# Performance work log

Measured on AMD Instinct MI355X. Metric: run time of the kernel, lower is better.

The kernel has to match this reference:

```python
import jax, jax.numpy as jnp
import numpy as np

KERNEL_SIZE = 5


def setup_inputs() -> dict:
    key = jax.random.key(0)
    k1, k2 = jax.random.split(key)
    x = jax.random.normal(k1, (4, 32, 256, 256), dtype=jnp.float32)
    kernel = jax.random.normal(k2, (4, KERNEL_SIZE * KERNEL_SIZE, 256, 256), dtype=jnp.float32)
    return {"x": x, "kernel": kernel}


def reference(x, kernel):
    k = KERNEL_SIZE
    b, kk, h, w = kernel.shape
    # softmax over the k*k dim (original permutes to channels-last then softmax dim=-1)
    kern = jax.nn.softmax(jnp.transpose(kernel, (0, 2, 3, 1)), axis=-1)  # [b,h,w,k*k]
    pad = (k - 1) // 2
    # replicate padding on spatial dims
    xp = jnp.pad(x, ((0, 0), (0, 0), (pad, pad), (pad, pad)), mode="edge")
    # unfold: patch index order is di*k + dj (height offset first), matching torch unfold(2).unfold(3)
    patches = jnp.stack(
        [xp[:, :, i:i + h, j:j + w] for i in range(k) for j in range(k)], axis=-1
    )  # [b,c,h,w,k*k]
    # per-pixel softmax-weighted local sum; kernel broadcast over channel dim
    out = jnp.sum(patches * kern[:, None, :, :, :], axis=-1)  # [b,c,h,w]
    return out
```

## Files before the change

### kernel.cpp

```cpp
#include <hip/hip_runtime.h>

#define HW    256
#define HW2   (HW*HW)
#define KTAPS 25
#define TW    32
#define TH    4
#define LW    36
#define LH    8
#define NEL   (LW*LH)
#define NSTG  5
#define BUFSZ (NSTG*64)
#define NRING 4
#define DEPTH 2
#define CPB   8
#define C     32

__device__ __forceinline__ void stage(const float* __restrict__ src, float* dst,
                                      const int* __restrict__ soff) {
#pragma unroll
    for (int k = 0; k < NSTG; ++k)
        __builtin_amdgcn_global_load_lds(
            (const __attribute__((address_space(1))) unsigned int*)(src + soff[k]),
            (__attribute__((address_space(3))) unsigned int*)(dst + k * 64),
            4, 0, 0);
}

__global__ __launch_bounds__(64, 5) void ddown_kernel(
    const float* __restrict__ x,
    const float* __restrict__ kern,
    float* __restrict__ out)
{
    __shared__ __align__(16) float xt[NRING][BUFSZ];

    const int lane = threadIdx.x;
    const int txq  = lane & 15;
    const int ty   = lane >> 4;
    const int w0   = blockIdx.x * TW;
    const int h0   = blockIdx.y * TH;
    const int b    = blockIdx.z >> 2;
    const int c0   = (blockIdx.z & 3) * CPB;

    const int h = h0 + ty;
    const int w = w0 + txq * 2;

    const float* xb = x + (size_t)(b * C + c0) * HW2;

    int soff[NSTG];
#pragma unroll
    for (int k = 0; k < NSTG; ++k) {
        int idx = lane + k * 64;
        int i   = idx / LW;
        int j   = idx - i * LW;
        int hh  = min(max(h0 + i - 2, 0), HW - 1);
        int ww  = min(max(w0 + j - 2, 0), HW - 1);
        soff[k] = hh * HW + ww;
    }

    stage(xb,       xt[0], soff);
    stage(xb + HW2, xt[1], soff);

    const float* kb = kern + (size_t)b * KTAPS * HW2 + h * HW + w;
    float2 wt[KTAPS];
    float sx = 0.f, sy = 0.f;
#pragma unroll
    for (int j = 0; j < KTAPS; ++j) {
        float2 v = *(const float2*)(kb + (size_t)j * HW2);
        v.x = __expf(v.x); v.y = __expf(v.y);
        sx += v.x; sy += v.y;
        wt[j] = v;
    }
    const float ix = 1.f / sx, iy = 1.f / sy;

    float* ob = out + (size_t)(b * C + c0) * HW2 + h * HW + w;

#pragma unroll
    for (int cc = 0; cc < CPB; ++cc) {
        if (cc + DEPTH < CPB) stage(xb + (size_t)(cc + DEPTH) * HW2, xt[(cc + DEPTH) % NRING], soff);

        if (cc < 6)       asm volatile("s_waitcnt vmcnt(10)" ::: "memory");
        else if (cc == 6) asm volatile("s_waitcnt vmcnt(5)"  ::: "memory");
        else              asm volatile("s_waitcnt vmcnt(0)"  ::: "memory");

        const float* xc = xt[cc % NRING];
        float ax = 0.f, ay = 0.f;
#pragma unroll
        for (int di = 0; di < 5; ++di) {
            const float* row = &xc[(ty + di) * LW + txq * 2];
            float2 pa = *(const float2*)(row);
            float2 pb = *(const float2*)(row + 2);
            float2 pc = *(const float2*)(row + 4);
            float w6[6] = {pa.x, pa.y, pb.x, pb.y, pc.x, pc.y};
#pragma unroll
            for (int dj = 0; dj < 5; ++dj) {
                float2 wv = wt[di * 5 + dj];
                ax += wv.x * w6[dj + 0];
                ay += wv.y * w6[dj + 1];
            }
        }
        float2 res = { ax * ix, ay * iy };
        *(float2*)(ob + (size_t)cc * HW2) = res;
    }
}

extern "C" void kernel_launch(void* const* d_in, const int* in_sizes, int n_in,
                              void* d_out, int out_size, void* d_ws, size_t ws_size,
                              hipStream_t stream) {
    const float* x    = (const float*)d_in[0];
    const float* kern = (const float*)d_in[1];
    float* out        = (float*)d_out;

    dim3 grid(HW / TW, HW / TH, 4 * 4);
    ddown_kernel<<<grid, 64, 0, stream>>>(x, kern, out);
}
```

Baseline: 114.4 us.

## Use 16-byte global-to-LDS loads for interior tiles and double channels per block

Interior column blocks now stage the padded halo tile with two 16-byte global_load_lds calls per lane instead of five 4-byte ones, using a 40-wide aligned LDS row. Edge blocks keep the clamped scalar path through a templated channel loop. Each block now handles 16 channels instead of 8, so the softmax weights are computed half as often, and the waitcnt schedules are retuned for each path. The cost is a larger LDS footprint, lower occupancy (launch bounds 5 to 4), half as many blocks, and two code paths with hand-counted vmcnt values that must stay correct.

```diff
diff --git a/kernel.cpp b/kernel.cpp
--- a/kernel.cpp
+++ b/kernel.cpp
@@ -5,87 +5,66 @@
 #define KTAPS 25
 #define TW    32
 #define TH    4
-#define LW    36
+#define LW    40
 #define LH    8
 #define NEL   (LW*LH)
-#define NSTG  5
-#define BUFSZ (NSTG*64)
+#define BUFSZ 512
 #define NRING 4
 #define DEPTH 2
-#define CPB   8
+#define CPB   16
 #define C     32
 
-__device__ __forceinline__ void stage(const float* __restrict__ src, float* dst,
-                                      const int* __restrict__ soff) {
+__device__ __forceinline__ void stage4(const float* __restrict__ src, float* dst,
+                                       const int* __restrict__ soff4) {
 #pragma unroll
-    for (int k = 0; k < NSTG; ++k)
+    for (int k = 0; k < 2; ++k)
+        __builtin_amdgcn_global_load_lds(
+            (const __attribute__((address_space(1))) unsigned int*)(src + soff4[k]),
+            (__attribute__((address_space(3))) unsigned int*)(dst + k * 256),
+            16, 0, 0);
+}
+
+__device__ __forceinline__ void stage1(const float* __restrict__ src, float* dst,
+                                       const int* __restrict__ soff) {
+#pragma unroll
+    for (int k = 0; k < 5; ++k)
         __builtin_amdgcn_global_load_lds(
             (const __attribute__((address_space(1))) unsigned int*)(src + soff[k]),
             (__attribute__((address_space(3))) unsigned int*)(dst + k * 64),
             4, 0, 0);
 }
 
-__global__ __launch_bounds__(64, 5) void ddown_kernel(
-    const float* __restrict__ x,
-    const float* __restrict__ kern,
-    float* __restrict__ out)
+template <int NL>
+__device__ __forceinline__ void channel_loop(
+    const float* __restrict__ xb, float (*xt)[BUFSZ], const int* __restrict__ soff,
+    const float2* __restrict__ wt, float ix, float iy,
+    float* __restrict__ ob, int ty, int txq)
 {
-    __shared__ __align__(16) float xt[NRING][BUFSZ];
-
-    const int lane = threadIdx.x;
-    const int txq  = lane & 15;
-    const int ty   = lane >> 4;
-    const int w0   = blockIdx.x * TW;
-    const int h0   = blockIdx.y * TH;
-    const int b    = blockIdx.z >> 2;
-    const int c0   = (blockIdx.z & 3) * CPB;
-
-    const int h = h0 + ty;
-    const int w = w0 + txq * 2;
-
-    const float* xb = x + (size_t)(b * C + c0) * HW2;
-
-    int soff[NSTG];
-#pragma unroll
-    for (int k = 0; k < NSTG; ++k) {
-        int idx = lane + k * 64;
-        int i   = idx / LW;
-        int j   = idx - i * LW;
-        int hh  = min(max(h0 + i - 2, 0), HW - 1);
-        int ww  = min(max(w0 + j - 2, 0), HW - 1);
-        soff[k] = hh * HW + ww;
-    }
-
-    stage(xb,       xt[0], soff);
-    stage(xb + HW2, xt[1], soff);
-
-    const float* kb = kern + (size_t)b * KTAPS * HW2 + h * HW + w;
-    float2 wt[KTAPS];
-    float sx = 0.f, sy = 0.f;
-#pragma unroll
-    for (int j = 0; j < KTAPS; ++j) {
-        float2 v = *(const float2*)(kb + (size_t)j * HW2);
-        v.x = __expf(v.x); v.y = __expf(v.y);
-        sx += v.x; sy += v.y;
-        wt[j] = v;
-    }
-    const float ix = 1.f / sx, iy = 1.f / sy;
-
-    float* ob = out + (size_t)(b * C + c0) * HW2 + h * HW + w;
-
 #pragma unroll
     for (int cc = 0; cc < CPB; ++cc) {
-        if (cc + DEPTH < CPB) stage(xb + (size_t)(cc + DEPTH) * HW2, xt[(cc + DEPTH) % NRING], soff);
-
-        if (cc < 6)       asm volatile("s_waitcnt vmcnt(10)" ::: "memory");
-        else if (cc == 6) asm volatile("s_waitcnt vmcnt(5)"  ::: "memory");
-        else              asm volatile("s_waitcnt vmcnt(0)"  ::: "memory");
+        if (cc + DEPTH < CPB) {
+            if constexpr (NL == 2)
+                stage4(xb + (size_t)(cc + DEPTH) * HW2, xt[(cc + DEPTH) % NRING], soff);
+            else
+                stage1(xb + (size_t)(cc + DEPTH) * HW2, xt[(cc + DEPTH) % NRING], soff);
+        }
+        if constexpr (NL == 2) {
+            if      (cc <= 1)  asm volatile("s_waitcnt vmcnt(29)" ::: "memory");
+            else if (cc <= 13) asm volatile("s_waitcnt vmcnt(4)"  ::: "memory");
+            else if (cc == 14) asm volatile("s_waitcnt vmcnt(2)"  ::: "memory");
+            else               asm volatile("s_waitcnt vmcnt(0)"  ::: "memory");
+        } else {
+            if      (cc <= 1)  asm volatile("s_waitcnt vmcnt(35)" ::: "memory");
+            else if (cc <= 13) asm volatile("s_waitcnt vmcnt(10)" ::: "memory");
+            else if (cc == 14) asm volatile("s_waitcnt vmcnt(5)"  ::: "memory");
+            else               asm volatile("s_waitcnt vmcnt(0)"  ::: "memory");
+        }
 
         const float* xc = xt[cc % NRING];
         float ax = 0.f, ay = 0.f;
 #pragma unroll
         for (int di = 0; di < 5; ++di) {
-            const float* row = &xc[(ty + di) * LW + txq * 2];
+            const float* row = &xc[(ty + di) * LW + txq * 2 + 2];
             float2 pa = *(const float2*)(row);
             float2 pb = *(const float2*)(row + 2);
             float2 pc = *(const float2*)(row + 4);
@@ -102,6 +81,71 @@
     }
 }
 
+__global__ __launch_bounds__(64, 4) void ddown_kernel(
+    const float* __restrict__ x,
+    const float* __restrict__ kern,
+    float* __restrict__ out)
+{
+    __shared__ __align__(16) float xt[NRING][BUFSZ];
+
+    const int lane = threadIdx.x;
+    const int txq  = lane & 15;
+    const int ty   = lane >> 4;
+    const int w0   = blockIdx.x * TW;
+    const int h0   = blockIdx.y * TH;
+    const int b    = blockIdx.z >> 1;
+    const int c0   = (blockIdx.z & 1) * CPB;
+
+    const int h = h0 + ty;
+    const int w = w0 + txq * 2;
+
+    const float* xb = x + (size_t)(b * C + c0) * HW2;
+    const bool interior = (blockIdx.x >= 1) && (blockIdx.x <= 6);
+
+    int soff[5];
+    if (interior) {
+#pragma unroll
+        for (int k = 0; k < 2; ++k) {
+            int m  = k * 64 + lane;
+            int i  = m / 10;
+            int j4 = 4 * (m - i * 10);
+            int hh = min(max(h0 + i - 2, 0), HW - 1);
+            soff[k] = hh * HW + (w0 + j4 - 4);
+        }
+        stage4(xb,       xt[0], soff);
+        stage4(xb + HW2, xt[1], soff);
+    } else {
+#pragma unroll
+        for (int k = 0; k < 5; ++k) {
+            int idx = lane + k * 64;
+            int i   = idx / LW;
+            int j   = idx - i * LW;
+            int hh  = min(max(h0 + i - 2, 0), HW - 1);
+            int ww  = min(max(w0 + j - 4, 0), HW - 1);
+            soff[k] = hh * HW + ww;
+        }
+        stage1(xb,       xt[0], soff);
+        stage1(xb + HW2, xt[1], soff);
+    }
+
+    const float* kb = kern + (size_t)b * KTAPS * HW2 + h * HW + w;
+    float2 wt[KTAPS];
+    float sx = 0.f, sy = 0.f;
+#pragma unroll
+    for (int j = 0; j < KTAPS; ++j) {
+        float2 v = *(const float2*)(kb + (size_t)j * HW2);
+        v.x = __expf(v.x); v.y = __expf(v.y);
+        sx += v.x; sy += v.y;
+        wt[j] = v;
+    }
+    const float ix = 1.f / sx, iy = 1.f / sy;
+
+    float* ob = out + (size_t)(b * C + c0) * HW2 + h * HW + w;
+
+    if (interior) channel_loop<2>(xb, xt, soff, wt, ix, iy, ob, ty, txq);
+    else          channel_loop<5>(xb, xt, soff, wt, ix, iy, ob, ty, txq);
+}
+
 extern "C" void kernel_launch(void* const* d_in, const int* in_sizes, int n_in,
                               void* d_out, int out_size, void* d_ws, size_t ws_size,
                               hipStream_t stream) {
@@ -109,6 +153,6 @@
     const float* kern = (const float*)d_in[1];
     float* out        = (float*)d_out;
 
-    dim3 grid(HW / TW, HW / TH, 4 * 4);
+    dim3 grid(HW / TW, HW / TH, 4 * 2);
     ddown_kernel<<<grid, 64, 0, stream>>>(x, kern, out);
 }
```

Result: no change. 113.0 us (-1.3%).
